# Optimization experiments

Measured on AMD Instinct MI355X. Metric: run time of the kernel, lower is better.

The kernel has to match this reference:

```python
import jax, jax.numpy as jnp
import numpy as np
from jax import lax

MEL = 80
HID = 512
NCLS = 64
B = 16
T = 1000


def setup_inputs() -> dict:
    key = jax.random.key(0)
    ks = jax.random.split(key, 16)
    s_in = 1.0 / np.sqrt(MEL)
    s_h = 1.0 / np.sqrt(HID)
    return {
        'feats': jax.random.normal(ks[0], (B, T, MEL), jnp.float32),
        'C0': jax.random.normal(ks[1], (MEL, HID), jnp.float32) * s_h,
        'B0': jax.random.normal(ks[2], (HID, MEL), jnp.float32) * s_in,
        'W0': jax.random.normal(ks[3], (HID, MEL), jnp.float32) * s_in,
        'a0': jax.random.normal(ks[4], (HID,), jnp.float32) * 0.1,
        'tau00': jnp.array([0.5], jnp.float32),
        'gamma0': jnp.array([0.25], jnp.float32),
        'C1': jax.random.normal(ks[5], (HID, HID), jnp.float32) * s_h,
        'B1': jax.random.normal(ks[6], (HID, HID), jnp.float32) * s_h,
        'W1': jax.random.normal(ks[7], (HID, HID), jnp.float32) * s_h,
        'a1': jax.random.normal(ks[8], (HID,), jnp.float32) * 0.1,
        'tau01': jnp.array([0.5], jnp.float32),
        'gamma1': jnp.array([0.25], jnp.float32),
        'head_w': jax.random.normal(ks[9], (NCLS, 2 * HID), jnp.float32) * (1.0 / np.sqrt(2 * HID)),
        'head_b': jnp.zeros((NCLS,), jnp.float32),
    }


def _cell_step(h, x_t, C, Bm, Wm, a, tau0, gamma):
    # x_t: (B, in_dim), h: (B, HID)
    x_scale = jnp.maximum(jnp.linalg.norm(x_t, axis=-1, keepdims=True), 1e-6)  # (B,1)
    x_norm = jnp.clip(x_t / x_scale, -1.0, 1.0)
    hd = lax.stop_gradient(h)
    error = x_t - jnp.tanh(hd @ C.T) * x_scale                                 # (B, in_dim)
    rel_err = jnp.minimum(jnp.linalg.norm(error, axis=-1) / lax.stop_gradient(x_scale[:, 0]), 4.0)
    surprise = jax.nn.sigmoid((rel_err - tau0[0]) / gamma[0])                   # (B,)
    base_eff = x_norm @ Bm.T                                                    # (B, HID)
    err_eff = error @ Wm.T                                                      # (B, HID)
    input_h = hd * 0.2 + base_eff * 0.6 + err_eff * surprise[:, None] * 0.2
    # liquid-time-constant update: surprise-gated leaky integration toward tanh(input_h)
    g = surprise[:, None] * jax.nn.sigmoid(a)[None, :]                          # (B, HID) in (0,1)
    h_new = h * (1.0 - g) + jnp.tanh(input_h) * g
    return h_new, base_eff


def reference(feats, C0, B0, W0, a0, tau00, gamma0, C1, B1, W1, a1, tau01, gamma1, head_w, head_b):
    Bsz = feats.shape[0]
    feats_t = jnp.swapaxes(feats, 0, 1)  # (T, B, MEL)
    h0_init = jnp.zeros((Bsz, HID), feats.dtype)
    h1_init = jnp.zeros((Bsz, HID), feats.dtype)

    def scan_fn(carry, x_t):
        h0, h1 = carry
        h0n, be0 = _cell_step(h0, x_t, C0, B0, W0, a0, tau00, gamma0)
        h1n, be1 = _cell_step(h1, be0, C1, B1, W1, a1, tau01, gamma1)
        return (h0n, h1n), jnp.concatenate([h1n, be1], axis=-1)

    _, ys = lax.scan(scan_fn, (h0_init, h1_init), feats_t)  # (T, B, 2*HID)
    stacked = jnp.swapaxes(ys, 0, 1)                        # (B, T, 2*HID)
    return stacked @ head_w.T + head_b                      # (B, T, NCLS)
```

## Files before the change

### kernel.cpp

```cpp
#include <hip/hip_runtime.h>
#include <math.h>

#define T_LEN 1000
#define BATCH 16
#define MEL   80
#define HID   512
#define NCLS  64
#define SL    8

__device__ __forceinline__ float fast_tanh(float x) {
    float e = __expf(2.0f * x);
    return 1.0f - 2.0f / (e + 1.0f);
}
__device__ __forceinline__ float fast_sigmoid(float x) {
    return 1.0f / (1.0f + __expf(-x));
}

__device__ __forceinline__ unsigned long long pack_pair(float v, unsigned e) {
    return ((unsigned long long)e << 32) | (unsigned long long)__float_as_uint(v);
}
__device__ __forceinline__ float pair_val(unsigned long long p) {
    return __uint_as_float((unsigned)(p & 0xffffffffull));
}
__device__ __forceinline__ unsigned pair_epoch(unsigned long long p) {
    return (unsigned)(p >> 32);
}

__device__ __forceinline__ void llc_load16c(const float* base, float4 (&r)[16]) {
    asm volatile(
        "global_load_dwordx4 %0, %16, off sc0 sc1\n\t"
        "global_load_dwordx4 %1, %16, off offset:16 sc0 sc1\n\t"
        "global_load_dwordx4 %2, %16, off offset:32 sc0 sc1\n\t"
        "global_load_dwordx4 %3, %16, off offset:48 sc0 sc1\n\t"
        "global_load_dwordx4 %4, %16, off offset:64 sc0 sc1\n\t"
        "global_load_dwordx4 %5, %16, off offset:80 sc0 sc1\n\t"
        "global_load_dwordx4 %6, %16, off offset:96 sc0 sc1\n\t"
        "global_load_dwordx4 %7, %16, off offset:112 sc0 sc1\n\t"
        "global_load_dwordx4 %8, %16, off offset:128 sc0 sc1\n\t"
        "global_load_dwordx4 %9, %16, off offset:144 sc0 sc1\n\t"
        "global_load_dwordx4 %10, %16, off offset:160 sc0 sc1\n\t"
        "global_load_dwordx4 %11, %16, off offset:176 sc0 sc1\n\t"
        "global_load_dwordx4 %12, %16, off offset:192 sc0 sc1\n\t"
        "global_load_dwordx4 %13, %16, off offset:208 sc0 sc1\n\t"
        "global_load_dwordx4 %14, %16, off offset:224 sc0 sc1\n\t"
        "global_load_dwordx4 %15, %16, off offset:240 sc0 sc1\n\t"
        "s_waitcnt vmcnt(0)"
        : "=&v"(r[0]), "=&v"(r[1]), "=&v"(r[2]), "=&v"(r[3]),
          "=&v"(r[4]), "=&v"(r[5]), "=&v"(r[6]), "=&v"(r[7]),
          "=&v"(r[8]), "=&v"(r[9]), "=&v"(r[10]), "=&v"(r[11]),
          "=&v"(r[12]), "=&v"(r[13]), "=&v"(r[14]), "=&v"(r[15])
        : "v"(base)
        : "memory");
}

__global__ void k0_init(unsigned long long* part) {
    int i = blockIdx.x * 256 + threadIdx.x;
    if (i < BATCH * 2 * SL * HID) part[i] = 0ull;
}

__global__ __launch_bounds__(256) void k1_be0(const float* __restrict__ feats,
                                              const float* __restrict__ B0,
                                              float* __restrict__ be0) {
    const int t = blockIdx.x;
    const int tid = threadIdx.x;
    __shared__ float xf[BATCH][MEL];
    __shared__ float sc[BATCH];
    for (int idx = tid; idx < BATCH * MEL; idx += 256) {
        int b = idx / MEL, m = idx % MEL;
        xf[b][m] = feats[b * (T_LEN * MEL) + t * MEL + m];
    }
    __syncthreads();
    if (tid < BATCH) {
        float ss = 0.f;
        for (int m = 0; m < MEL; ++m) { float v = xf[tid][m]; ss += v * v; }
        sc[tid] = fmaxf(sqrtf(ss), 1e-6f);
    }
    __syncthreads();
    for (int idx = tid; idx < BATCH * MEL; idx += 256) {
        int b = idx / MEL, m = idx % MEL;
        float v = xf[b][m] / sc[b];
        xf[b][m] = fminf(fmaxf(v, -1.f), 1.f);
    }
    __syncthreads();
    for (int j = tid; j < HID; j += 256) {
        float acc[BATCH];
        #pragma unroll
        for (int b = 0; b < BATCH; ++b) acc[b] = 0.f;
        const float* brow = B0 + j * MEL;
        for (int k = 0; k < MEL; k += 4) {
            float4 w = *(const float4*)(brow + k);
            #pragma unroll
            for (int b = 0; b < BATCH; ++b) {
                float4 xv = *(const float4*)(&xf[b][k]);
                acc[b] += w.x * xv.x + w.y * xv.y + w.z * xv.z + w.w * xv.w;
            }
        }
        #pragma unroll
        for (int b = 0; b < BATCH; ++b)
            be0[(t * BATCH + b) * HID + j] = acc[b];
    }
}

__global__ __launch_bounds__(256) void k2_be1(const float* __restrict__ be0,
                                              const float* __restrict__ B1,
                                              float* __restrict__ be1,
                                              float* __restrict__ xs1) {
    const int t = blockIdx.x;
    const int tid = threadIdx.x;
    __shared__ float xn[BATCH][HID];
    __shared__ float sc[BATCH];
    __shared__ float psum[BATCH][16];
    for (int idx = tid; idx < BATCH * HID; idx += 256) {
        int b = idx >> 9, k = idx & 511;
        xn[b][k] = be0[(t * BATCH + b) * HID + k];
    }
    __syncthreads();
    {
        int b = tid >> 4, l = tid & 15;
        float ss = 0.f;
        for (int k = l; k < HID; k += 16) { float v = xn[b][k]; ss += v * v; }
        psum[b][l] = ss;
    }
    __syncthreads();
    if (tid < BATCH) {
        float ss = 0.f;
        #pragma unroll
        for (int l = 0; l < 16; ++l) ss += psum[tid][l];
        float s = fmaxf(sqrtf(ss), 1e-6f);
        sc[tid] = s;
        xs1[t * BATCH + tid] = s;
    }
    __syncthreads();
    for (int idx = tid; idx < BATCH * HID; idx += 256) {
        int b = idx >> 9, k = idx & 511;
        float v = xn[b][k] / sc[b];
        xn[b][k] = fminf(fmaxf(v, -1.f), 1.f);
    }
    __syncthreads();
    for (int j = tid; j < HID; j += 256) {
        float acc[BATCH];
        #pragma unroll
        for (int b = 0; b < BATCH; ++b) acc[b] = 0.f;
        const float* brow = B1 + j * HID;
        for (int k = 0; k < HID; k += 4) {
            float4 w = *(const float4*)(brow + k);
            #pragma unroll
            for (int b = 0; b < BATCH; ++b) {
                float4 xv = *(const float4*)(&xn[b][k]);
                acc[b] += w.x * xv.x + w.y * xv.y + w.z * xv.z + w.w * xv.w;
            }
        }
        #pragma unroll
        for (int b = 0; b < BATCH; ++b)
            be1[(t * BATCH + b) * HID + j] = acc[b];
    }
}

__global__ __launch_bounds__(512, 1) void k3_fused(
    const float* __restrict__ be0, const float* __restrict__ be1,
    const float* __restrict__ xs1,
    const float* __restrict__ C1, const float* __restrict__ W1,
    const float* __restrict__ a1, const float* __restrict__ tau,
    const float* __restrict__ gam,
    float* __restrict__ h1s,
    unsigned long long* part)
{
    const int chain = blockIdx.x & 15;
    const int slice = blockIdx.x >> 4;
    const int tid = threadIdx.x;
    const int w = tid >> 6;
    const int lane = tid & 63;
    const int jq = tid >> 3;
    const int kc = tid & 7;
    const int j2 = slice * 64 + jq;
    const bool lead = (kc == 0);

    float4 wC[16], wW[16];
    llc_load16c(C1 + (size_t)tid * HID + slice * 64, wC);
    llc_load16c(W1 + (size_t)j2 * HID + kc * 64, wW);

    const float tauv = tau[0], gamv = gam[0];
    const float siga = fast_sigmoid(a1[j2]);

    unsigned long long* pc = part + (size_t)chain * (2 * SL * HID);

    __shared__ float h_s[64];
    __shared__ float e_s[HID + 32];
    __shared__ float sq_s[8];

    float hj = 0.f;
    if (tid < 64) h_s[tid] = 0.f;

    float cur_be0 = be0[(size_t)chain * HID + tid];
    float cur_be1 = 0.f;
    if (lead) cur_be1 = __builtin_nontemporal_load(&be1[(size_t)chain * HID + j2]);
    float cur_xs = xs1[chain];
    __syncthreads();

    for (int t = 0; t < T_LEN; ++t) {
        float nxt_be0 = 0.f, nxt_be1 = 0.f, nxt_xs = 0.f;
        if (t + 1 < T_LEN) {
            const size_t nrow = (size_t)((t + 1) * BATCH + chain) * HID;
            nxt_be0 = be0[nrow + tid];
            if (lead) nxt_be1 = __builtin_nontemporal_load(&be1[nrow + j2]);
            nxt_xs = xs1[(t + 1) * BATCH + chain];
        }
        const unsigned tag = (unsigned)(t + 1);
        unsigned long long* ps = pc + (size_t)(t & 1) * (SL * HID);

        {
            float p0 = 0.f, p1 = 0.f, p2 = 0.f, p3 = 0.f;
            #pragma unroll
            for (int i = 0; i < 16; ++i) {
                float4 hv = *(const float4*)(h_s + 4 * i);
                p0 += wC[i].x * hv.x; p1 += wC[i].y * hv.y;
                p2 += wC[i].z * hv.z; p3 += wC[i].w * hv.w;
            }
            float dpp = (p0 + p1) + (p2 + p3);
            __hip_atomic_store(&ps[slice * HID + tid], pack_pair(dpp, tag),
                               __ATOMIC_RELAXED, __HIP_MEMORY_SCOPE_AGENT);
        }

        float dp;
        {
            unsigned long long pv0, pv1, pv2, pv3, pv4, pv5, pv6, pv7;
            for (;;) {
                pv0 = __hip_atomic_load(&ps[0 * HID + tid], __ATOMIC_RELAXED, __HIP_MEMORY_SCOPE_AGENT);
                pv1 = __hip_atomic_load(&ps[1 * HID + tid], __ATOMIC_RELAXED, __HIP_MEMORY_SCOPE_AGENT);
                pv2 = __hip_atomic_load(&ps[2 * HID + tid], __ATOMIC_RELAXED, __HIP_MEMORY_SCOPE_AGENT);
                pv3 = __hip_atomic_load(&ps[3 * HID + tid], __ATOMIC_RELAXED, __HIP_MEMORY_SCOPE_AGENT);
                pv4 = __hip_atomic_load(&ps[4 * HID + tid], __ATOMIC_RELAXED, __HIP_MEMORY_SCOPE_AGENT);
                pv5 = __hip_atomic_load(&ps[5 * HID + tid], __ATOMIC_RELAXED, __HIP_MEMORY_SCOPE_AGENT);
                pv6 = __hip_atomic_load(&ps[6 * HID + tid], __ATOMIC_RELAXED, __HIP_MEMORY_SCOPE_AGENT);
                pv7 = __hip_atomic_load(&ps[7 * HID + tid], __ATOMIC_RELAXED, __HIP_MEMORY_SCOPE_AGENT);
                bool ok = (pair_epoch(pv0) == tag) & (pair_epoch(pv1) == tag)
                        & (pair_epoch(pv2) == tag) & (pair_epoch(pv3) == tag)
                        & (pair_epoch(pv4) == tag) & (pair_epoch(pv5) == tag)
                        & (pair_epoch(pv6) == tag) & (pair_epoch(pv7) == tag);
                if (__all(ok)) break;
                __builtin_amdgcn_s_sleep(1);
            }
            dp = ((pair_val(pv0) + pair_val(pv1)) + (pair_val(pv2) + pair_val(pv3)))
               + ((pair_val(pv4) + pair_val(pv5)) + (pair_val(pv6) + pair_val(pv7)));
        }

        {
            float err = cur_be0 - fast_tanh(dp) * cur_xs;
            e_s[tid + (tid >> 6) * 4] = err;
            float sq = err * err;
            #pragma unroll
            for (int off = 32; off > 0; off >>= 1) sq += __shfl_down(sq, off, 64);
            if (lane == 0) sq_s[w] = sq;
        }
        __syncthreads();

        {
            float ssT = ((sq_s[0] + sq_s[1]) + (sq_s[2] + sq_s[3]))
                      + ((sq_s[4] + sq_s[5]) + (sq_s[6] + sq_s[7]));
            const float* esb = e_s + kc * 68;
            float q0 = 0.f, q1 = 0.f, q2 = 0.f, q3 = 0.f;
            #pragma unroll
            for (int i = 0; i < 16; ++i) {
                float4 ev = *(const float4*)(esb + 4 * i);
                q0 += wW[i].x * ev.x; q1 += wW[i].y * ev.y;
                q2 += wW[i].z * ev.z; q3 += wW[i].w * ev.w;
            }
            float ee = (q0 + q1) + (q2 + q3);
            ee += __shfl_down(ee, 4, 8);
            ee += __shfl_down(ee, 2, 8);
            ee += __shfl_down(ee, 1, 8);
            if (lead) {
                float rel = fminf(sqrtf(ssT) / cur_xs, 4.0f);
                float s = fast_sigmoid((rel - tauv) / gamv);
                float input_h = hj * 0.2f + cur_be1 * 0.6f + ee * s * 0.2f;
                float g = s * siga;
                hj = hj * (1.f - g) + fast_tanh(input_h) * g;
                h_s[jq] = hj;
                __builtin_nontemporal_store(hj,
                    &h1s[(size_t)(t * BATCH + chain) * HID + j2]);
            }
        }
        __syncthreads();

        cur_be0 = nxt_be0; cur_be1 = nxt_be1; cur_xs = nxt_xs;
    }
}

__global__ __launch_bounds__(1024) void k4_head(const float* __restrict__ h1s,
                                                const float* __restrict__ be1,
                                                const float* __restrict__ head_w,
                                                const float* __restrict__ head_b,
                                                float* __restrict__ out) {
    const int t = blockIdx.x;
    const int tid = threadIdx.x;
    const int c = tid >> 4;
    const int b = tid & 15;
    const float* hw = head_w + c * (2 * HID);
    const float* x1 = h1s + (size_t)(t * BATCH + b) * HID;
    const float* x2 = be1 + (size_t)(t * BATCH + b) * HID;
    float acc0 = head_b[c], acc1 = 0.f;
    for (int k = 0; k < HID; k += 4) {
        float4 w = *(const float4*)(hw + k);
        float4 xv = *(const float4*)(x1 + k);
        acc0 += w.x * xv.x + w.y * xv.y + w.z * xv.z + w.w * xv.w;
    }
    for (int k = 0; k < HID; k += 4) {
        float4 w = *(const float4*)(hw + HID + k);
        float4 xv = *(const float4*)(x2 + k);
        acc1 += w.x * xv.x + w.y * xv.y + w.z * xv.z + w.w * xv.w;
    }
    out[b * (T_LEN * NCLS) + t * NCLS + c] = acc0 + acc1;
}

extern "C" void kernel_launch(void* const* d_in, const int* in_sizes, int n_in,
                              void* d_out, int out_size, void* d_ws, size_t ws_size,
                              hipStream_t stream) {
    const float* feats  = (const float*)d_in[0];
    const float* B0     = (const float*)d_in[2];
    const float* C1     = (const float*)d_in[7];
    const float* B1     = (const float*)d_in[8];
    const float* W1     = (const float*)d_in[9];
    const float* a1     = (const float*)d_in[10];
    const float* tau1   = (const float*)d_in[11];
    const float* gam1   = (const float*)d_in[12];
    const float* head_w = (const float*)d_in[13];
    const float* head_b = (const float*)d_in[14];
    float* out = (float*)d_out;

    float* be0 = (float*)d_ws;
    float* be1 = be0 + (size_t)T_LEN * BATCH * HID;
    float* xs1 = be1 + (size_t)T_LEN * BATCH * HID;
    float* h1s = xs1 + (size_t)T_LEN * BATCH;
    unsigned long long* part =
        (unsigned long long*)(h1s + (size_t)T_LEN * BATCH * HID);

    hipLaunchKernelGGL(k0_init, dim3(512), dim3(256), 0, stream, part);
    hipLaunchKernelGGL(k1_be0, dim3(T_LEN), dim3(256), 0, stream, feats, B0, be0);
    hipLaunchKernelGGL(k2_be1, dim3(T_LEN), dim3(256), 0, stream, be0, B1, be1, xs1);
    hipLaunchKernelGGL(k3_fused, dim3(BATCH * SL), dim3(512), 0, stream,
                       be0, be1, xs1, C1, W1, a1, tau1, gam1, h1s, part);
    hipLaunchKernelGGL(k4_head, dim3(T_LEN), dim3(1024), 0, stream,
                       h1s, be1, head_w, head_b, out);
}
```

Measured before the change: 4.342 ms.

## Replace per-element epoch-tagged partials with per-wave flag synchronization

Cross-block partial sums were exchanged as 64-bit value+epoch pairs, and every thread polled eight tagged words. They are now stored as plain 32-bit floats plus one flag per wave (64 flags per chain). Waiters poll only the flag array, then read the partials once. The prefetch of the next timestep's inputs moves after the partial publish so the store/flag signal goes out earlier. This cuts polling traffic and partial bandwidth, but adds a vmcnt wait and a second dependent load round after the flag check, and relies on relaxed-ordering visibility between the data stores and the flag store.

After: 7.967 ms. 1.83x slower.

```diff
diff --git a/kernel.cpp b/kernel.cpp
--- a/kernel.cpp
+++ b/kernel.cpp
@@ -14,16 +14,6 @@
 }
 __device__ __forceinline__ float fast_sigmoid(float x) {
     return 1.0f / (1.0f + __expf(-x));
-}
-
-__device__ __forceinline__ unsigned long long pack_pair(float v, unsigned e) {
-    return ((unsigned long long)e << 32) | (unsigned long long)__float_as_uint(v);
-}
-__device__ __forceinline__ float pair_val(unsigned long long p) {
-    return __uint_as_float((unsigned)(p & 0xffffffffull));
-}
-__device__ __forceinline__ unsigned pair_epoch(unsigned long long p) {
-    return (unsigned)(p >> 32);
 }
 
 __device__ __forceinline__ void llc_load16c(const float* base, float4 (&r)[16]) {
@@ -53,9 +43,9 @@
         : "memory");
 }
 
-__global__ void k0_init(unsigned long long* part) {
+__global__ void k0_init(unsigned* flags) {
     int i = blockIdx.x * 256 + threadIdx.x;
-    if (i < BATCH * 2 * SL * HID) part[i] = 0ull;
+    if (i < BATCH * 2 * 64) flags[i] = 0u;
 }
 
 __global__ __launch_bounds__(256) void k1_be0(const float* __restrict__ feats,
@@ -163,7 +153,7 @@
     const float* __restrict__ a1, const float* __restrict__ tau,
     const float* __restrict__ gam,
     float* __restrict__ h1s,
-    unsigned long long* part)
+    float* __restrict__ pvals, unsigned* __restrict__ flags)
 {
     const int chain = blockIdx.x & 15;
     const int slice = blockIdx.x >> 4;
@@ -182,10 +172,8 @@
     const float tauv = tau[0], gamv = gam[0];
     const float siga = fast_sigmoid(a1[j2]);
 
-    unsigned long long* pc = part + (size_t)chain * (2 * SL * HID);
-
     __shared__ float h_s[64];
-    __shared__ float e_s[HID + 32];
+    __shared__ __align__(16) float e_s[HID + 32];
     __shared__ float sq_s[8];
 
     float hj = 0.f;
@@ -198,6 +186,28 @@
     __syncthreads();
 
     for (int t = 0; t < T_LEN; ++t) {
+        const unsigned tag = (unsigned)(t + 1);
+        float*    pv = pvals + ((size_t)chain * 2 + (t & 1)) * (SL * HID);
+        unsigned* fl = flags + ((size_t)chain * 2 + (t & 1)) * 64;
+
+        {
+            float p0 = 0.f, p1 = 0.f, p2 = 0.f, p3 = 0.f;
+            #pragma unroll
+            for (int i = 0; i < 16; ++i) {
+                float4 hv = *(const float4*)(h_s + 4 * i);
+                p0 += wC[i].x * hv.x; p1 += wC[i].y * hv.y;
+                p2 += wC[i].z * hv.z; p3 += wC[i].w * hv.w;
+            }
+            float pp = (p0 + p1) + (p2 + p3);
+            __hip_atomic_store((unsigned*)&pv[slice * HID + tid],
+                               __float_as_uint(pp),
+                               __ATOMIC_RELAXED, __HIP_MEMORY_SCOPE_AGENT);
+        }
+        asm volatile("s_waitcnt vmcnt(0)" ::: "memory");
+        if (lane == 0)
+            __hip_atomic_store(&fl[slice * 8 + w], tag,
+                               __ATOMIC_RELAXED, __HIP_MEMORY_SCOPE_AGENT);
+
         float nxt_be0 = 0.f, nxt_be1 = 0.f, nxt_xs = 0.f;
         if (t + 1 < T_LEN) {
             const size_t nrow = (size_t)((t + 1) * BATCH + chain) * HID;
@@ -205,43 +215,23 @@
             if (lead) nxt_be1 = __builtin_nontemporal_load(&be1[nrow + j2]);
             nxt_xs = xs1[(t + 1) * BATCH + chain];
         }
-        const unsigned tag = (unsigned)(t + 1);
-        unsigned long long* ps = pc + (size_t)(t & 1) * (SL * HID);
 
         {
-            float p0 = 0.f, p1 = 0.f, p2 = 0.f, p3 = 0.f;
-            #pragma unroll
-            for (int i = 0; i < 16; ++i) {
-                float4 hv = *(const float4*)(h_s + 4 * i);
-                p0 += wC[i].x * hv.x; p1 += wC[i].y * hv.y;
-                p2 += wC[i].z * hv.z; p3 += wC[i].w * hv.w;
-            }
-            float dpp = (p0 + p1) + (p2 + p3);
-            __hip_atomic_store(&ps[slice * HID + tid], pack_pair(dpp, tag),
-                               __ATOMIC_RELAXED, __HIP_MEMORY_SCOPE_AGENT);
-        }
-
-        float dp;
-        {
-            unsigned long long pv0, pv1, pv2, pv3, pv4, pv5, pv6, pv7;
+            unsigned fv;
             for (;;) {
-                pv0 = __hip_atomic_load(&ps[0 * HID + tid], __ATOMIC_RELAXED, __HIP_MEMORY_SCOPE_AGENT);
-                pv1 = __hip_atomic_load(&ps[1 * HID + tid], __ATOMIC_RELAXED, __HIP_MEMORY_SCOPE_AGENT);
-                pv2 = __hip_atomic_load(&ps[2 * HID + tid], __ATOMIC_RELAXED, __HIP_MEMORY_SCOPE_AGENT);
-                pv3 = __hip_atomic_load(&ps[3 * HID + tid], __ATOMIC_RELAXED, __HIP_MEMORY_SCOPE_AGENT);
-                pv4 = __hip_atomic_load(&ps[4 * HID + tid], __ATOMIC_RELAXED, __HIP_MEMORY_SCOPE_AGENT);
-                pv5 = __hip_atomic_load(&ps[5 * HID + tid], __ATOMIC_RELAXED, __HIP_MEMORY_SCOPE_AGENT);
-                pv6 = __hip_atomic_load(&ps[6 * HID + tid], __ATOMIC_RELAXED, __HIP_MEMORY_SCOPE_AGENT);
-                pv7 = __hip_atomic_load(&ps[7 * HID + tid], __ATOMIC_RELAXED, __HIP_MEMORY_SCOPE_AGENT);
-                bool ok = (pair_epoch(pv0) == tag) & (pair_epoch(pv1) == tag)
-                        & (pair_epoch(pv2) == tag) & (pair_epoch(pv3) == tag)
-                        & (pair_epoch(pv4) == tag) & (pair_epoch(pv5) == tag)
-                        & (pair_epoch(pv6) == tag) & (pair_epoch(pv7) == tag);
-                if (__all(ok)) break;
+                fv = __hip_atomic_load(&fl[lane], __ATOMIC_RELAXED,
+                                       __HIP_MEMORY_SCOPE_AGENT);
+                if (__all(fv == tag)) break;
                 __builtin_amdgcn_s_sleep(1);
             }
-            dp = ((pair_val(pv0) + pair_val(pv1)) + (pair_val(pv2) + pair_val(pv3)))
-               + ((pair_val(pv4) + pair_val(pv5)) + (pair_val(pv6) + pair_val(pv7)));
+        }
+
+        float dp = 0.f;
+        #pragma unroll
+        for (int p = 0; p < SL; ++p) {
+            unsigned u = __hip_atomic_load((const unsigned*)&pv[p * HID + tid],
+                                           __ATOMIC_RELAXED, __HIP_MEMORY_SCOPE_AGENT);
+            dp += __uint_as_float(u);
         }
 
         {
@@ -331,14 +321,15 @@
     float* be1 = be0 + (size_t)T_LEN * BATCH * HID;
     float* xs1 = be1 + (size_t)T_LEN * BATCH * HID;
     float* h1s = xs1 + (size_t)T_LEN * BATCH;
-    unsigned long long* part =
-        (unsigned long long*)(h1s + (size_t)T_LEN * BATCH * HID);
-
-    hipLaunchKernelGGL(k0_init, dim3(512), dim3(256), 0, stream, part);
+    float* pvals = h1s + (size_t)T_LEN * BATCH * HID;
+    unsigned* flags =
+        (unsigned*)(pvals + (size_t)BATCH * 2 * SL * HID);
+
+    hipLaunchKernelGGL(k0_init, dim3(8), dim3(256), 0, stream, flags);
     hipLaunchKernelGGL(k1_be0, dim3(T_LEN), dim3(256), 0, stream, feats, B0, be0);
     hipLaunchKernelGGL(k2_be1, dim3(T_LEN), dim3(256), 0, stream, be0, B1, be1, xs1);
     hipLaunchKernelGGL(k3_fused, dim3(BATCH * SL), dim3(512), 0, stream,
-                       be0, be1, xs1, C1, W1, a1, tau1, gam1, h1s, part);
+                       be0, be1, xs1, C1, W1, a1, tau1, gam1, h1s, pvals, flags);
     hipLaunchKernelGGL(k4_head, dim3(T_LEN), dim3(1024), 0, stream,
                        h1s, be1, head_w, head_b, out);
 }
```

## Split be1 precompute into norm kernel and register-tiled GEMM over timestep tiles

Applied to the files above, without the earlier changes.

Splits the old k2_be1 kernel in two. The first kernel computes the per-timestep input norm with a shuffle reduction. The second kernel keeps a 64-row slice of B1 in registers and reuses it across a tile of 8 timesteps, splitting each output's dot product across 4 lanes, so B1 is no longer reread from global memory for every timestep. It also moves the next-step prefetch in the recurrent kernel to after the spin-wait, and aligns a shared buffer. The cost is one extra launch and heavier register use, and the recurrent kernel probably dominates total time anyway.

Result: slower. 4.542 ms (+4.6%).

```diff
diff --git a/kernel.cpp b/kernel.cpp
--- a/kernel.cpp
+++ b/kernel.cpp
@@ -7,6 +7,7 @@
 #define HID   512
 #define NCLS  64
 #define SL    8
+#define TT2   8
 
 __device__ __forceinline__ float fast_tanh(float x) {
     float e = __expf(2.0f * x);
@@ -101,58 +102,74 @@
     }
 }
 
-__global__ __launch_bounds__(256) void k2_be1(const float* __restrict__ be0,
-                                              const float* __restrict__ B1,
-                                              float* __restrict__ be1,
+__global__ __launch_bounds__(256) void k2a_xs(const float* __restrict__ be0,
                                               float* __restrict__ xs1) {
     const int t = blockIdx.x;
     const int tid = threadIdx.x;
-    __shared__ float xn[BATCH][HID];
-    __shared__ float sc[BATCH];
-    __shared__ float psum[BATCH][16];
-    for (int idx = tid; idx < BATCH * HID; idx += 256) {
-        int b = idx >> 9, k = idx & 511;
-        xn[b][k] = be0[(t * BATCH + b) * HID + k];
-    }
-    __syncthreads();
-    {
-        int b = tid >> 4, l = tid & 15;
-        float ss = 0.f;
-        for (int k = l; k < HID; k += 16) { float v = xn[b][k]; ss += v * v; }
-        psum[b][l] = ss;
-    }
-    __syncthreads();
-    if (tid < BATCH) {
-        float ss = 0.f;
+    const int b = tid >> 4, l = tid & 15;
+    const float* row = be0 + ((size_t)t * BATCH + b) * HID;
+    float ss = 0.f;
+    for (int k = l * 4; k < HID; k += 64) {
+        float4 v = *(const float4*)(row + k);
+        ss += v.x * v.x + v.y * v.y + v.z * v.z + v.w * v.w;
+    }
+    ss += __shfl_down(ss, 8, 16);
+    ss += __shfl_down(ss, 4, 16);
+    ss += __shfl_down(ss, 2, 16);
+    ss += __shfl_down(ss, 1, 16);
+    if (l == 0) xs1[t * BATCH + b] = fmaxf(sqrtf(ss), 1e-6f);
+}
+
+__global__ __launch_bounds__(256, 2) void k2b_gemm(const float* __restrict__ be0,
+                                                   const float* __restrict__ B1,
+                                                   const float* __restrict__ xs1,
+                                                   float* __restrict__ be1) {
+    const int tile = blockIdx.x >> 3;
+    const int slice = blockIdx.x & 7;
+    const int tid = threadIdx.x;
+    const int j = tid >> 2, kc = tid & 3;
+    const int jg = slice * 64 + j;
+
+    float4 wA[16], wB[16];
+    const float* wb = B1 + (size_t)jg * HID + kc * 128;
+    llc_load16c(wb, wA);
+    llc_load16c(wb + 64, wB);
+
+    __shared__ float xn[BATCH][528];
+    __shared__ float scs[BATCH];
+
+    for (int tt = 0; tt < TT2; ++tt) {
+        const int t = tile * TT2 + tt;
+        if (tid < BATCH) scs[tid] = xs1[t * BATCH + tid];
+        __syncthreads();
+        for (int idx = tid; idx < BATCH * HID; idx += 256) {
+            int b = idx >> 9, k = idx & 511;
+            float v = be0[((size_t)t * BATCH + b) * HID + k] / scs[b];
+            xn[b][k + (k >> 7) * 4] = fminf(fmaxf(v, -1.f), 1.f);
+        }
+        __syncthreads();
         #pragma unroll
-        for (int l = 0; l < 16; ++l) ss += psum[tid][l];
-        float s = fmaxf(sqrtf(ss), 1e-6f);
-        sc[tid] = s;
-        xs1[t * BATCH + tid] = s;
-    }
-    __syncthreads();
-    for (int idx = tid; idx < BATCH * HID; idx += 256) {
-        int b = idx >> 9, k = idx & 511;
-        float v = xn[b][k] / sc[b];
-        xn[b][k] = fminf(fmaxf(v, -1.f), 1.f);
-    }
-    __syncthreads();
-    for (int j = tid; j < HID; j += 256) {
-        float acc[BATCH];
-        #pragma unroll
-        for (int b = 0; b < BATCH; ++b) acc[b] = 0.f;
-        const float* brow = B1 + j * HID;
-        for (int k = 0; k < HID; k += 4) {
-            float4 w = *(const float4*)(brow + k);
-            #pragma unroll
-            for (int b = 0; b < BATCH; ++b) {
-                float4 xv = *(const float4*)(&xn[b][k]);
-                acc[b] += w.x * xv.x + w.y * xv.y + w.z * xv.z + w.w * xv.w;
-            }
-        }
-        #pragma unroll
-        for (int b = 0; b < BATCH; ++b)
-            be1[(t * BATCH + b) * HID + j] = acc[b];
+        for (int b = 0; b < BATCH; ++b) {
+            const float* xb = &xn[b][kc * 132];
+            float a0 = 0.f, a1 = 0.f, a2 = 0.f, a3 = 0.f;
+            #pragma unroll
+            for (int i = 0; i < 16; ++i) {
+                float4 xv = *(const float4*)(xb + 4 * i);
+                a0 += wA[i].x * xv.x; a1 += wA[i].y * xv.y;
+                a2 += wA[i].z * xv.z; a3 += wA[i].w * xv.w;
+            }
+            #pragma unroll
+            for (int i = 0; i < 16; ++i) {
+                float4 xv = *(const float4*)(xb + 64 + 4 * i);
+                a0 += wB[i].x * xv.x; a1 += wB[i].y * xv.y;
+                a2 += wB[i].z * xv.z; a3 += wB[i].w * xv.w;
+            }
+            float v = (a0 + a1) + (a2 + a3);
+            v += __shfl_down(v, 2, 4);
+            v += __shfl_down(v, 1, 4);
+            if (kc == 0) be1[((size_t)t * BATCH + b) * HID + jg] = v;
+        }
+        __syncthreads();
     }
 }
 
@@ -185,7 +202,7 @@
     unsigned long long* pc = part + (size_t)chain * (2 * SL * HID);
 
     __shared__ float h_s[64];
-    __shared__ float e_s[HID + 32];
+    __shared__ __align__(16) float e_s[HID + 32];
     __shared__ float sq_s[8];
 
     float hj = 0.f;
@@ -198,13 +215,6 @@
     __syncthreads();
 
     for (int t = 0; t < T_LEN; ++t) {
-        float nxt_be0 = 0.f, nxt_be1 = 0.f, nxt_xs = 0.f;
-        if (t + 1 < T_LEN) {
-            const size_t nrow = (size_t)((t + 1) * BATCH + chain) * HID;
-            nxt_be0 = be0[nrow + tid];
-            if (lead) nxt_be1 = __builtin_nontemporal_load(&be1[nrow + j2]);
-            nxt_xs = xs1[(t + 1) * BATCH + chain];
-        }
         const unsigned tag = (unsigned)(t + 1);
         unsigned long long* ps = pc + (size_t)(t & 1) * (SL * HID);
 
@@ -216,8 +226,8 @@
                 p0 += wC[i].x * hv.x; p1 += wC[i].y * hv.y;
                 p2 += wC[i].z * hv.z; p3 += wC[i].w * hv.w;
             }
-            float dpp = (p0 + p1) + (p2 + p3);
-            __hip_atomic_store(&ps[slice * HID + tid], pack_pair(dpp, tag),
+            float pp = (p0 + p1) + (p2 + p3);
+            __hip_atomic_store(&ps[slice * HID + tid], pack_pair(pp, tag),
                                __ATOMIC_RELAXED, __HIP_MEMORY_SCOPE_AGENT);
         }
 
@@ -244,6 +254,14 @@
                + ((pair_val(pv4) + pair_val(pv5)) + (pair_val(pv6) + pair_val(pv7)));
         }
 
+        float nxt_be0 = 0.f, nxt_be1 = 0.f, nxt_xs = 0.f;
+        if (t + 1 < T_LEN) {
+            const size_t nrow = (size_t)((t + 1) * BATCH + chain) * HID;
+            nxt_be0 = be0[nrow + tid];
+            if (lead) nxt_be1 = __builtin_nontemporal_load(&be1[nrow + j2]);
+            nxt_xs = xs1[(t + 1) * BATCH + chain];
+        }
+
         {
             float err = cur_be0 - fast_tanh(dp) * cur_xs;
             e_s[tid + (tid >> 6) * 4] = err;
@@ -336,7 +354,9 @@
 
     hipLaunchKernelGGL(k0_init, dim3(512), dim3(256), 0, stream, part);
     hipLaunchKernelGGL(k1_be0, dim3(T_LEN), dim3(256), 0, stream, feats, B0, be0);
-    hipLaunchKernelGGL(k2_be1, dim3(T_LEN), dim3(256), 0, stream, be0, B1, be1, xs1);
+    hipLaunchKernelGGL(k2a_xs, dim3(T_LEN), dim3(256), 0, stream, be0, xs1);
+    hipLaunchKernelGGL(k2b_gemm, dim3((T_LEN / TT2) * 8), dim3(256), 0, stream,
+                       be0, B1, xs1, be1);
     hipLaunchKernelGGL(k3_fused, dim3(BATCH * SL), dim3(512), 0, stream,
                        be0, be1, xs1, C1, W1, a1, tau1, gam1, h1s, part);
     hipLaunchKernelGGL(k4_head, dim3(T_LEN), dim3(1024), 0, stream,
```
